# Kernel tuning notes

Hardware: AMD Instinct MI355X
Metric: run time of the kernel (lower is better)

Reference implementation:

```python
import jax, jax.numpy as jnp
import numpy as np

B, N, D, H, HD, C = 2, 2048, 2048, 16, 128, 128  # batch, seq, embed, heads, head_dim, chunk
EPS = 1e-6


def setup_inputs() -> dict:
    key = jax.random.key(0)
    ks = jax.random.split(key, 9)
    s = 0.02
    x = jax.random.normal(ks[0], (B, N, D), jnp.float32)
    # per-head negative log decay (lambda = exp(log_decay) in (0,1))
    log_decay = -jax.random.uniform(ks[1], (H,), jnp.float32, minval=0.01, maxval=1.0)
    Wq = jax.random.normal(ks[2], (D, D), jnp.float32) * s
    Wk = jax.random.normal(ks[3], (D, D), jnp.float32) * s
    Wv = jax.random.normal(ks[4], (D, D), jnp.float32) * s
    Wo = jax.random.normal(ks[5], (D, D), jnp.float32) * s
    Wg1 = jax.random.normal(ks[6], (D, HD), jnp.float32) * s
    Wg2 = jax.random.normal(ks[7], (HD, D), jnp.float32) * s
    norm_w = jnp.ones((D,), jnp.float32)
    return dict(x=x, log_decay=log_decay, Wq=Wq, Wk=Wk, Wv=Wv, Wo=Wo,
                Wg1=Wg1, Wg2=Wg2, norm_w=norm_w)


def _lasd(q, k, v, ld):
    # causal linear attention with per-head scalar log-decay, chunked scan.
    # q,k,v: [B,N,H,HD]; ld: [H] (negative). Recurrence: S_t = exp(ld)*S_{t-1} + k_t v_t^T; o_t = q_t @ S_t
    nc = N // C
    to_chunks = lambda t: t.reshape(B, nc, C, H, HD).transpose(1, 0, 3, 2, 4)  # [nc,B,H,C,HD]
    qc, kc, vc = map(to_chunks, (q, k, v))
    i = jnp.arange(C, dtype=jnp.float32)
    diff = i[:, None] - i[None, :]                     # [C,C]
    Dm = jnp.exp(jnp.where(diff >= 0, ld[:, None, None] * diff, -jnp.inf))  # [H,C,C]
    dq = jnp.exp(ld[:, None] * (i + 1.0))              # [H,C] decay applied to q vs chunk-start state
    dk = jnp.exp(ld[:, None] * (C - 1.0 - i))          # [H,C] decay applied to k for state update
    dS = jnp.exp(ld * C)                               # [H]   chunk-level state decay

    def step(S, qkv):
        qb, kb, vb = qkv                               # [B,H,C,HD]
        attn = jnp.einsum('bhid,bhjd->bhij', qb, kb) * Dm
        o = jnp.einsum('bhij,bhje->bhie', attn, vb)
        o = o + jnp.einsum('bhid,bhde->bhie', qb * dq[None, :, :, None], S)
        S = S * dS[None, :, None, None] + jnp.einsum('bhjd,bhje->bhde', kb * dk[None, :, :, None], vb)
        return S, o

    S0 = jnp.zeros((B, H, HD, HD), jnp.float32)
    _, o = jax.lax.scan(step, S0, (qc, kc, vc))        # [nc,B,H,C,HD]
    return o.transpose(1, 0, 3, 2, 4).reshape(B, N, H, HD)


def reference(x, log_decay, Wq, Wk, Wv, Wo, Wg1, Wg2, norm_w):
    silu = jax.nn.silu
    q = silu(x @ Wq).reshape(B, N, H, HD)
    k = silu(x @ Wk).reshape(B, N, H, HD)
    v = silu(x @ Wv).reshape(B, N, H, HD)
    o = _lasd(q, k, v, log_decay).reshape(B, N, D)
    gate = jax.nn.sigmoid((x @ Wg1) @ Wg2)             # two stacked linears, no nonlinearity between
    o = o * gate
    o = o * jax.lax.rsqrt(jnp.mean(o * o, axis=-1, keepdims=True) + EPS) * norm_w  # rmsnorm
    return o @ Wo
```

## Files before the change

kernel.cpp:

```cpp
#include <hip/hip_runtime.h>
#include <hip/hip_bf16.h>
#include <cstdint>
#include <cstddef>

#define B_   2
#define N_   2048
#define D_   2048
#define H_   16
#define HD_  128
#define C_   128
#define NC_  16
#define M_   4096
#define QKVG_ 8192

typedef __attribute__((ext_vector_type(8))) short bf16x8;
typedef __attribute__((ext_vector_type(4))) float f32x4;
typedef __attribute__((ext_vector_type(16))) float f32x16;

__device__ __forceinline__ uint16_t f2bf(float f){
  __hip_bfloat16 h = __float2bfloat16(f);
  return *reinterpret_cast<uint16_t*>(&h);
}
__device__ __forceinline__ float bf2f(uint16_t u){
  union { uint32_t i; float f; } v; v.i = ((uint32_t)u) << 16; return v.f;
}

__device__ __forceinline__ void async16(const uint16_t* g, uint16_t* l){
  __builtin_amdgcn_global_load_lds(
      (const __attribute__((address_space(1))) void*)g,
      (__attribute__((address_space(3))) void*)l, 16, 0, 0);
}

__device__ __forceinline__ int swz(int row, int c){
  return row*128 + ((((c >> 3) ^ row) & 15) << 3) + (c & 7);
}

__global__ __launch_bounds__(256) void cast_kernel(
    const float* __restrict__ x, uint16_t* __restrict__ y)
{
  int i = (blockIdx.x*256 + threadIdx.x)*4;
  float4 f = *(const float4*)(x + i);
  ushort4 u;
  u.x = f2bf(f.x); u.y = f2bf(f.y); u.z = f2bf(f.z); u.w = f2bf(f.w);
  *(ushort4*)(y + i) = u;
}

__global__ __launch_bounds__(256)
void prep_weights(const float* __restrict__ Wq, const float* __restrict__ Wk,
                  const float* __restrict__ Wv, const float* __restrict__ Wo,
                  const float* __restrict__ Wg2, const float* __restrict__ Wg1,
                  uint16_t* __restrict__ WT, uint16_t* __restrict__ WoT,
                  uint16_t* __restrict__ Wg2T, uint16_t* __restrict__ Wg1b)
{
  const int z = blockIdx.z;
  const int tx = threadIdx.x & 31;
  const int ty = threadIdx.x >> 5;
  __shared__ uint16_t tile[32][33];

  if (z == 5){
    if (blockIdx.x >= 4) return;
    const int r0 = blockIdx.y*32, c0 = blockIdx.x*32;
    #pragma unroll
    for (int rr = 0; rr < 4; ++rr){
      int r = r0 + ty + rr*8;
      Wg1b[(size_t)r*HD_ + c0 + tx] = f2bf(Wg1[(size_t)r*HD_ + c0 + tx]);
    }
    return;
  }

  const float* src; uint16_t* dst; int R, Cc;
  if (z < 3)      { src = (z==0)?Wq:(z==1)?Wk:Wv; dst = WT + (size_t)z*D_*D_; R = D_; Cc = D_; }
  else if (z == 3){ src = Wo;  dst = WoT;  R = D_;  Cc = D_; }
  else            { if (blockIdx.y >= 4) return;
                    src = Wg2; dst = Wg2T; R = HD_; Cc = D_; }

  const int r0 = blockIdx.y*32, c0 = blockIdx.x*32;
  #pragma unroll
  for (int rr = 0; rr < 4; ++rr){
    int r = ty + rr*8;
    tile[r][tx] = f2bf(src[(size_t)(r0 + r)*Cc + c0 + tx]);
  }
  __syncthreads();
  #pragma unroll
  for (int rr = 0; rr < 4; ++rr){
    int r = ty + rr*8;
    dst[(size_t)(c0 + r)*R + r0 + tx] = tile[tx][r];
  }
}

template<int ACT, int OUTBF>
__global__ __launch_bounds__(256)
void gemm_bt2(const uint16_t* __restrict__ A, const uint16_t* __restrict__ Bt,
              void* __restrict__ Cout, int M, int Ncols, int K, int klen)
{
  __shared__ __align__(16) uint16_t As[128*64];
  __shared__ __align__(16) uint16_t Bs[128*64];
  const int t    = threadIdx.x;
  const int lane = t & 63, wave = t >> 6;
  const int wm = wave >> 1, wn = wave & 1;
  const int row0 = wm*64, col0 = wn*64;
  const int lm = lane & 31, lh = lane >> 5;

  const uint16_t* Ap = A  + (size_t)(blockIdx.y*128)*K;
  const uint16_t* Bp = Bt + (size_t)(blockIdx.x*128)*K;
  const int kbeg = blockIdx.z * klen;

  f32x16 acc[2][2];
  #pragma unroll
  for (int i = 0; i < 2; ++i)
    #pragma unroll
    for (int j = 0; j < 2; ++j)
      #pragma unroll
      for (int r = 0; r < 16; ++r) acc[i][j][r] = 0.f;

  const int srow = t >> 3;
  const int gch  = (t & 7) ^ (srow & 7);
  const size_t aoff0 = (size_t)srow*K + gch*8;

  for (int k0 = kbeg; k0 < kbeg + klen; k0 += 64){
    #pragma unroll
    for (int c = 0; c < 4; ++c){
      async16(Ap + (size_t)(c*32)*K + aoff0 + k0, As + c*2048 + t*8);
      async16(Bp + (size_t)(c*32)*K + aoff0 + k0, Bs + c*2048 + t*8);
    }
    __syncthreads();
    #pragma unroll
    for (int kh = 0; kh < 4; ++kh){
      bf16x8 af[2], bfr[2];
      const int ch = kh*2 + lh;
      #pragma unroll
      for (int i = 0; i < 2; ++i){
        int r = row0 + i*32 + lm;
        af[i] = *(const bf16x8*)(As + r*64 + ((ch ^ (r & 7)) << 3));
      }
      #pragma unroll
      for (int j = 0; j < 2; ++j){
        int r = col0 + j*32 + lm;
        bfr[j] = *(const bf16x8*)(Bs + r*64 + ((ch ^ (r & 7)) << 3));
      }
      #pragma unroll
      for (int i = 0; i < 2; ++i)
        #pragma unroll
        for (int j = 0; j < 2; ++j)
          acc[i][j] = __builtin_amdgcn_mfma_f32_32x32x16_bf16(af[i], bfr[j], acc[i][j], 0, 0, 0);
    }
    __syncthreads();
  }

  const int mode = (ACT == 3) ? ((blockIdx.x < 48) ? 1 : 2) : ACT;
  uint16_t* outb = (uint16_t*)Cout;
  float*    outf = (float*)Cout + (OUTBF ? 0 : (size_t)blockIdx.z*M*Ncols);
  #pragma unroll
  for (int i = 0; i < 2; ++i){
    #pragma unroll
    for (int j = 0; j < 2; ++j){
      #pragma unroll
      for (int r = 0; r < 16; ++r){
        int row = blockIdx.y*128 + row0 + i*32 + (r & 3) + 8*(r >> 2) + 4*lh;
        int col = blockIdx.x*128 + col0 + j*32 + lm;
        float v = acc[i][j][r];
        if (mode == 1)      v = v / (1.f + __expf(-v));
        else if (mode == 2) v = 1.f / (1.f + __expf(-v));
        size_t off = (size_t)row*Ncols + col;
        if (OUTBF) outb[off] = f2bf(v);
        else       outf[off] = v;
      }
    }
  }
}

__global__ __launch_bounds__(256)
void add_kernel(const float* __restrict__ p0, const float* __restrict__ p1,
                float* __restrict__ out)
{
  int i = (blockIdx.x*256 + threadIdx.x)*4;
  float4 a = *(const float4*)(p0 + i);
  float4 b = *(const float4*)(p1 + i);
  float4 o; o.x = a.x+b.x; o.y = a.y+b.y; o.z = a.z+b.z; o.w = a.w+b.w;
  *(float4*)(out + i) = o;
}

__global__ __launch_bounds__(256)
void chunk_state_kernel(const uint16_t* __restrict__ qkvg,
                        const float* __restrict__ log_decay, uint16_t* __restrict__ MsumT)
{
  __shared__ __align__(16) uint16_t vT[128*128];
  __shared__ __align__(16) uint16_t kT[128*128];
  const int h = blockIdx.x, b = blockIdx.y, ic = blockIdx.z;
  const int t    = threadIdx.x;
  const int lane = t & 63, wave = t >> 6;
  const int wm = wave >> 1, wn = wave & 1;
  const int e0 = wm*64, d0 = wn*64;
  const int lr = lane & 15, kq = lane >> 4;
  const float ld = log_decay[h];
  const size_t rowbase = (size_t)b*N_ + (size_t)ic*C_;
  const uint16_t* kb = qkvg + (size_t)D_;
  const uint16_t* vb = qkvg + (size_t)2*D_;

  #pragma unroll 4
  for (int it = 0; it < 64; ++it){
    int idx = t + it*256;
    int j = idx >> 7, e = idx & 127;
    uint16_t vv = vb[(rowbase + j)*QKVG_ + h*HD_ + e];
    float kf = bf2f(kb[(rowbase + j)*QKVG_ + h*HD_ + e]) * __expf(ld * (float)(C_ - 1 - j));
    vT[swz(e, j)] = vv;
    kT[swz(e, j)] = f2bf(kf);
  }
  __syncthreads();

  const f32x4 zero = {0.f, 0.f, 0.f, 0.f};
  f32x4 acc[4][4];
  #pragma unroll
  for (int i = 0; i < 4; ++i)
    #pragma unroll
    for (int j = 0; j < 4; ++j) acc[i][j] = zero;

  #pragma unroll
  for (int kt = 0; kt < 4; ++kt){
    bf16x8 af[4], bfr[4];
    #pragma unroll
    for (int i = 0; i < 4; ++i)
      af[i]  = *(const bf16x8*)(vT + swz(e0 + i*16 + lr, kt*32 + kq*8));
    #pragma unroll
    for (int j = 0; j < 4; ++j)
      bfr[j] = *(const bf16x8*)(kT + swz(d0 + j*16 + lr, kt*32 + kq*8));
    #pragma unroll
    for (int i = 0; i < 4; ++i)
      #pragma unroll
      for (int j = 0; j < 4; ++j)
        acc[i][j] = __builtin_amdgcn_mfma_f32_16x16x32_bf16(af[i], bfr[j], acc[i][j], 0, 0, 0);
  }

  uint16_t* Mout = MsumT + (((size_t)ic*B_ + b)*H_ + h)*(size_t)(HD_*HD_);
  #pragma unroll
  for (int i = 0; i < 4; ++i)
    #pragma unroll
    for (int j = 0; j < 4; ++j)
      #pragma unroll
      for (int r = 0; r < 4; ++r)
        Mout[(size_t)(e0 + i*16 + kq*4 + r)*HD_ + d0 + j*16 + lr] = f2bf(acc[i][j][r]);
}

__global__ __launch_bounds__(256)
void scan_kernel(const uint16_t* __restrict__ MsumT, const float* __restrict__ log_decay,
                 uint16_t* __restrict__ StT)
{
  const int h = blockIdx.x, b = blockIdx.y;
  const float ld = log_decay[h];
  const float dS = __expf(ld * (float)C_);
  const int base_e = blockIdx.z*2048;
  float cur[8];
  #pragma unroll
  for (int r = 0; r < 8; ++r) cur[r] = 0.f;
  for (int i = 0; i < NC_; ++i){
    const size_t base = (((size_t)i*B_ + b)*H_ + h)*(size_t)(HD_*HD_) + base_e;
    #pragma unroll
    for (int r = 0; r < 8; ++r){
      int idx = threadIdx.x + r*256;
      StT[base + idx] = f2bf(cur[r]);
      cur[r] = cur[r]*dS + bf2f(MsumT[base + idx]);
    }
  }
}

__global__ __launch_bounds__(256)
void attn_kernel(const uint16_t* __restrict__ qkvg, const uint16_t* __restrict__ StT,
                 const float* __restrict__ log_decay, float* __restrict__ o_attn)
{
  __shared__ __align__(16) uint16_t Ps[128*128];
  __shared__ __align__(16) uint16_t vT[128*128];
  const int h = blockIdx.x, b = blockIdx.y, ic = blockIdx.z;
  const int t    = threadIdx.x;
  const int lane = t & 63, wave = t >> 6;
  const int wm = wave >> 1, wn = wave & 1;
  const int row0 = wm*64, col0 = wn*64;
  const int lr = lane & 15, kq = lane >> 4;
  const float ld = log_decay[h];
  const size_t rowbase = (size_t)b*N_ + (size_t)ic*C_;
  const uint16_t* qb = qkvg;
  const uint16_t* kb = qkvg + (size_t)D_;
  const uint16_t* vb = qkvg + (size_t)2*D_;

  #pragma unroll 4
  for (int it = 0; it < 64; ++it){
    int idx = t + it*256;
    int j = idx >> 7, e = idx & 127;
    vT[swz(e, j)] = vb[(rowbase + j)*QKVG_ + h*HD_ + e];
  }

  const f32x4 zero = {0.f, 0.f, 0.f, 0.f};
  f32x4 acc[4][4];
  #pragma unroll
  for (int i = 0; i < 4; ++i)
    #pragma unroll
    for (int j = 0; j < 4; ++j) acc[i][j] = zero;

  #pragma unroll
  for (int kt = 0; kt < 4; ++kt){
    bf16x8 af[4], bfr[4];
    #pragma unroll
    for (int i = 0; i < 4; ++i)
      af[i]  = *(const bf16x8*)(qb + (rowbase + row0 + i*16 + lr)*QKVG_ + h*HD_ + kt*32 + kq*8);
    #pragma unroll
    for (int j = 0; j < 4; ++j)
      bfr[j] = *(const bf16x8*)(kb + (rowbase + col0 + j*16 + lr)*QKVG_ + h*HD_ + kt*32 + kq*8);
    #pragma unroll
    for (int i = 0; i < 4; ++i)
      #pragma unroll
      for (int j = 0; j < 4; ++j)
        acc[i][j] = __builtin_amdgcn_mfma_f32_16x16x32_bf16(af[i], bfr[j], acc[i][j], 0, 0, 0);
  }
  #pragma unroll
  for (int i = 0; i < 4; ++i)
    #pragma unroll
    for (int j = 0; j < 4; ++j)
      #pragma unroll
      for (int r = 0; r < 4; ++r){
        int row = row0 + i*16 + kq*4 + r;
        int col = col0 + j*16 + lr;
        int dlt = row - col;
        float f = (dlt >= 0) ? __expf(ld * (float)dlt) : 0.f;
        Ps[swz(row, col)] = f2bf(acc[i][j][r] * f);
      }

  #pragma unroll
  for (int i = 0; i < 4; ++i)
    #pragma unroll
    for (int j = 0; j < 4; ++j) acc[i][j] = zero;
  const uint16_t* Sb = StT + (((size_t)ic*B_ + b)*H_ + h)*(size_t)(HD_*HD_);
  #pragma unroll
  for (int kt = 0; kt < 4; ++kt){
    bf16x8 af[4], bfr[4];
    #pragma unroll
    for (int i = 0; i < 4; ++i)
      af[i]  = *(const bf16x8*)(qb + (rowbase + row0 + i*16 + lr)*QKVG_ + h*HD_ + kt*32 + kq*8);
    #pragma unroll
    for (int j = 0; j < 4; ++j)
      bfr[j] = *(const bf16x8*)(Sb + (size_t)(col0 + j*16 + lr)*HD_ + kt*32 + kq*8);
    #pragma unroll
    for (int i = 0; i < 4; ++i)
      #pragma unroll
      for (int j = 0; j < 4; ++j)
        acc[i][j] = __builtin_amdgcn_mfma_f32_16x16x32_bf16(af[i], bfr[j], acc[i][j], 0, 0, 0);
  }
  #pragma unroll
  for (int i = 0; i < 4; ++i)
    #pragma unroll
    for (int r = 0; r < 4; ++r){
      float dqv = __expf(ld * (float)(row0 + i*16 + kq*4 + r + 1));
      #pragma unroll
      for (int j = 0; j < 4; ++j) acc[i][j][r] *= dqv;
    }

  __syncthreads();

  #pragma unroll
  for (int kt = 0; kt < 4; ++kt){
    bf16x8 af[4], bfr[4];
    #pragma unroll
    for (int i = 0; i < 4; ++i)
      af[i]  = *(const bf16x8*)(Ps + swz(row0 + i*16 + lr, kt*32 + kq*8));
    #pragma unroll
    for (int j = 0; j < 4; ++j)
      bfr[j] = *(const bf16x8*)(vT + swz(col0 + j*16 + lr, kt*32 + kq*8));
    #pragma unroll
    for (int i = 0; i < 4; ++i)
      #pragma unroll
      for (int j = 0; j < 4; ++j)
        acc[i][j] = __builtin_amdgcn_mfma_f32_16x16x32_bf16(af[i], bfr[j], acc[i][j], 0, 0, 0);
  }

  #pragma unroll
  for (int i = 0; i < 4; ++i)
    #pragma unroll
    for (int j = 0; j < 4; ++j)
      #pragma unroll
      for (int r = 0; r < 4; ++r){
        int row = row0 + i*16 + kq*4 + r;
        int col = col0 + j*16 + lr;
        o_attn[(rowbase + row)*D_ + h*HD_ + col] = acc[i][j][r];
      }
}

__global__ __launch_bounds__(256)
void gate_norm_kernel(const float* __restrict__ o_attn, const uint16_t* __restrict__ qkvg,
                      const float* __restrict__ norm_w, uint16_t* __restrict__ on)
{
  const int row = blockIdx.x;
  const int t = threadIdx.x;
  const int c1 = t*4, c2 = 1024 + t*4;
  const float*    orow = o_attn + (size_t)row*D_;
  const uint16_t* grow = qkvg + (size_t)row*QKVG_ + 3*D_;
  float4  o1 = *(const float4*)(orow + c1);
  float4  o2 = *(const float4*)(orow + c2);
  ushort4 g1 = *(const ushort4*)(grow + c1);
  ushort4 g2 = *(const ushort4*)(grow + c2);
  float v[8];
  v[0] = o1.x*bf2f(g1.x); v[1] = o1.y*bf2f(g1.y); v[2] = o1.z*bf2f(g1.z); v[3] = o1.w*bf2f(g1.w);
  v[4] = o2.x*bf2f(g2.x); v[5] = o2.y*bf2f(g2.y); v[6] = o2.z*bf2f(g2.z); v[7] = o2.w*bf2f(g2.w);
  float s = 0.f;
  #pragma unroll
  for (int k = 0; k < 8; ++k) s += v[k]*v[k];
  #pragma unroll
  for (int off = 32; off > 0; off >>= 1) s += __shfl_down(s, off);
  __shared__ float red[4];
  if ((t & 63) == 0) red[t >> 6] = s;
  __syncthreads();
  float total = red[0] + red[1] + red[2] + red[3];
  float scale = rsqrtf(total * (1.f/(float)D_) + 1e-6f);
  float4 w1 = *(const float4*)(norm_w + c1);
  float4 w2 = *(const float4*)(norm_w + c2);
  ushort4 b1, b2;
  b1.x = f2bf(v[0]*scale*w1.x); b1.y = f2bf(v[1]*scale*w1.y);
  b1.z = f2bf(v[2]*scale*w1.z); b1.w = f2bf(v[3]*scale*w1.w);
  b2.x = f2bf(v[4]*scale*w2.x); b2.y = f2bf(v[5]*scale*w2.y);
  b2.z = f2bf(v[6]*scale*w2.z); b2.w = f2bf(v[7]*scale*w2.w);
  *(ushort4*)(on + (size_t)row*D_ + c1) = b1;
  *(ushort4*)(on + (size_t)row*D_ + c2) = b2;
}

extern "C" void kernel_launch(void* const* d_in, const int* in_sizes, int n_in,
                              void* d_out, int out_size, void* d_ws, size_t ws_size,
                              hipStream_t stream) {
  const float* x         = (const float*)d_in[0];
  const float* log_decay = (const float*)d_in[1];
  const float* Wq        = (const float*)d_in[2];
  const float* Wk        = (const float*)d_in[3];
  const float* Wv        = (const float*)d_in[4];
  const float* Wo        = (const float*)d_in[5];
  const float* Wg1       = (const float*)d_in[6];
  const float* Wg2       = (const float*)d_in[7];
  const float* norm_w    = (const float*)d_in[8];
  float* out = (float*)d_out;

  uint8_t* p = (uint8_t*)d_ws;
  uint16_t* xb    = (uint16_t*)p; p += (size_t)M_*D_*2;
  uint16_t* WT    = (uint16_t*)p; p += (size_t)QKVG_*D_*2;
  uint16_t* WoT   = (uint16_t*)p; p += (size_t)D_*D_*2;
  uint16_t* Wg1b  = (uint16_t*)p; p += (size_t)D_*HD_*2;
  uint16_t* Wg2T  = (uint16_t*)p; p += (size_t)D_*HD_*2;
  uint16_t* qkvg  = (uint16_t*)p; p += (size_t)M_*QKVG_*2;
  uint16_t* MsumT = (uint16_t*)p; p += (size_t)NC_*B_*H_*HD_*HD_*2;
  uint16_t* StT   = (uint16_t*)p; p += (size_t)NC_*B_*H_*HD_*HD_*2;
  float*    o_att = (float*)WT;
  uint16_t* on    = xb;
  float*    part  = (float*)qkvg;

  cast_kernel<<<(M_*D_)/1024, 256, 0, stream>>>(x, xb);
  prep_weights<<<dim3(64, 64, 6), 256, 0, stream>>>(Wq, Wk, Wv, Wo, Wg2, Wg1,
                                                    WT, WoT, Wg2T, Wg1b);

  gemm_bt2<0,1><<<dim3(D_/128, D_/128, 1), 256, 0, stream>>>(
      Wg2T, Wg1b, WT + (size_t)3*D_*D_, D_, D_, HD_, HD_);

  gemm_bt2<3,1><<<dim3(QKVG_/128, M_/128, 1), 256, 0, stream>>>(
      xb, WT, qkvg, M_, QKVG_, D_, D_);

  chunk_state_kernel<<<dim3(H_, B_, NC_), 256, 0, stream>>>(qkvg, log_decay, MsumT);
  scan_kernel<<<dim3(H_, B_, 8), 256, 0, stream>>>(MsumT, log_decay, StT);
  attn_kernel<<<dim3(H_, B_, NC_), 256, 0, stream>>>(qkvg, StT, log_decay, o_att);

  gate_norm_kernel<<<M_, 256, 0, stream>>>(o_att, qkvg, norm_w, on);
  gemm_bt2<0,0><<<dim3(D_/128, M_/128, 2), 256, 0, stream>>>(
      on, WoT, part, M_, D_, D_, D_/2);
  add_kernel<<<(M_*D_)/1024, 256, 0, stream>>>(part, part + (size_t)M_*D_, out);
}
```

Before: 426.3 us.

## Add 256x256-tile double-buffered GEMM and use it for QKVG and output projections

After: 480.2 us. 12.6% more time.

```diff
diff --git a/kernel.cpp b/kernel.cpp
--- a/kernel.cpp
+++ b/kernel.cpp
@@ -158,6 +158,128 @@
       for (int r = 0; r < 16; ++r){
         int row = blockIdx.y*128 + row0 + i*32 + (r & 3) + 8*(r >> 2) + 4*lh;
         int col = blockIdx.x*128 + col0 + j*32 + lm;
+        float v = acc[i][j][r];
+        if (mode == 1)      v = v / (1.f + __expf(-v));
+        else if (mode == 2) v = 1.f / (1.f + __expf(-v));
+        size_t off = (size_t)row*Ncols + col;
+        if (OUTBF) outb[off] = f2bf(v);
+        else       outf[off] = v;
+      }
+    }
+  }
+}
+
+template<int ACT, int OUTBF>
+__global__ __launch_bounds__(512, 2)
+void gemm256(const uint16_t* __restrict__ A, const uint16_t* __restrict__ Bt,
+             void* __restrict__ Cout, int M, int Ncols, int K, int klen)
+{
+  __shared__ __align__(16) uint16_t As[2*256*32];
+  __shared__ __align__(16) uint16_t Bs[2*256*32];
+  const int t    = threadIdx.x;
+  const int lane = t & 63, wave = t >> 6;
+  const int wm = wave >> 1, wn = wave & 1;
+  const int lm = lane & 31, lh = lane >> 5;
+  const int sl0 = (lh ^ (lm & 3)) << 3;
+  const int ar = wm*64  + lm;
+  const int br = wn*128 + lm;
+
+  const uint16_t* Ap = A  + (size_t)(blockIdx.y*256)*K;
+  const uint16_t* Bp = Bt + (size_t)(blockIdx.x*256)*K;
+  const int kbeg = blockIdx.z*klen;
+  const int NT   = klen >> 5;
+
+  const int r_lo = t >> 2;
+  const int gch  = (t & 3) ^ (r_lo & 3);
+  const size_t src0 = (size_t)r_lo*K + gch*8;
+  const size_t src1 = src0 + (size_t)128*K;
+  const int ldst = t*8;
+
+  f32x16 acc[2][4];
+  #pragma unroll
+  for (int i = 0; i < 2; ++i)
+    #pragma unroll
+    for (int j = 0; j < 4; ++j)
+      #pragma unroll
+      for (int r = 0; r < 16; ++r) acc[i][j][r] = 0.f;
+
+  async16(Ap + src0 + kbeg,      As + ldst);
+  async16(Ap + src1 + kbeg,      As + 4096 + ldst);
+  async16(Bp + src0 + kbeg,      Bs + ldst);
+  async16(Bp + src1 + kbeg,      Bs + 4096 + ldst);
+  async16(Ap + src0 + kbeg + 32, As + 8192 + ldst);
+  async16(Ap + src1 + kbeg + 32, As + 8192 + 4096 + ldst);
+  async16(Bp + src0 + kbeg + 32, Bs + 8192 + ldst);
+  async16(Bp + src1 + kbeg + 32, Bs + 8192 + 4096 + ldst);
+  asm volatile("s_waitcnt vmcnt(4)" ::: "memory");
+  __builtin_amdgcn_s_barrier();
+  asm volatile("" ::: "memory");
+
+  bf16x8 af0[2], bf0[4], af1[2], bf1[4];
+  #pragma unroll
+  for (int i = 0; i < 2; ++i) af0[i] = *(const bf16x8*)(As + (ar + i*32)*32 + sl0);
+  #pragma unroll
+  for (int j = 0; j < 4; ++j) bf0[j] = *(const bf16x8*)(Bs + (br + j*32)*32 + sl0);
+
+  for (int tt = 0; tt < NT; ++tt){
+    uint16_t* Ac = As + (tt & 1)*8192;
+    uint16_t* Bc = Bs + (tt & 1)*8192;
+    const uint16_t* An = As + ((tt & 1) ^ 1)*8192;
+    const uint16_t* Bn = Bs + ((tt & 1) ^ 1)*8192;
+
+    #pragma unroll
+    for (int i = 0; i < 2; ++i) af1[i] = *(const bf16x8*)(Ac + (ar + i*32)*32 + (sl0 ^ 16));
+    #pragma unroll
+    for (int j = 0; j < 4; ++j) bf1[j] = *(const bf16x8*)(Bc + (br + j*32)*32 + (sl0 ^ 16));
+    __builtin_amdgcn_s_setprio(1);
+    #pragma unroll
+    for (int i = 0; i < 2; ++i)
+      #pragma unroll
+      for (int j = 0; j < 4; ++j)
+        acc[i][j] = __builtin_amdgcn_mfma_f32_32x32x16_bf16(af0[i], bf0[j], acc[i][j], 0, 0, 0);
+    __builtin_amdgcn_s_setprio(0);
+    asm volatile("s_waitcnt lgkmcnt(0)" ::: "memory");
+    __builtin_amdgcn_s_barrier();
+    asm volatile("" ::: "memory");
+
+    if (tt + 2 < NT){
+      const size_t kc = (size_t)kbeg + (size_t)(tt + 2)*32;
+      async16(Ap + src0 + kc, Ac + ldst);
+      async16(Ap + src1 + kc, Ac + 4096 + ldst);
+      async16(Bp + src0 + kc, Bc + ldst);
+      async16(Bp + src1 + kc, Bc + 4096 + ldst);
+      asm volatile("s_waitcnt vmcnt(4)" ::: "memory");
+    } else {
+      asm volatile("s_waitcnt vmcnt(0)" ::: "memory");
+    }
+    __builtin_amdgcn_s_barrier();
+    asm volatile("" ::: "memory");
+    if (tt + 1 < NT){
+      #pragma unroll
+      for (int i = 0; i < 2; ++i) af0[i] = *(const bf16x8*)(An + (ar + i*32)*32 + sl0);
+      #pragma unroll
+      for (int j = 0; j < 4; ++j) bf0[j] = *(const bf16x8*)(Bn + (br + j*32)*32 + sl0);
+    }
+    __builtin_amdgcn_s_setprio(1);
+    #pragma unroll
+    for (int i = 0; i < 2; ++i)
+      #pragma unroll
+      for (int j = 0; j < 4; ++j)
+        acc[i][j] = __builtin_amdgcn_mfma_f32_32x32x16_bf16(af1[i], bf1[j], acc[i][j], 0, 0, 0);
+    __builtin_amdgcn_s_setprio(0);
+  }
+
+  const int mode = (ACT == 3) ? (((blockIdx.x << 8) < Ncols - 2048) ? 1 : 2) : ACT;
+  uint16_t* outb = (uint16_t*)Cout;
+  float*    outf = (float*)Cout + (OUTBF ? 0 : (size_t)blockIdx.z*M*Ncols);
+  #pragma unroll
+  for (int i = 0; i < 2; ++i){
+    #pragma unroll
+    for (int j = 0; j < 4; ++j){
+      #pragma unroll
+      for (int r = 0; r < 16; ++r){
+        int row = blockIdx.y*256 + wm*64  + i*32 + (r & 3) + 8*(r >> 2) + 4*lh;
+        int col = blockIdx.x*256 + wn*128 + j*32 + lm;
         float v = acc[i][j][r];
         if (mode == 1)      v = v / (1.f + __expf(-v));
         else if (mode == 2) v = 1.f / (1.f + __expf(-v));
@@ -453,7 +575,7 @@
   gemm_bt2<0,1><<<dim3(D_/128, D_/128, 1), 256, 0, stream>>>(
       Wg2T, Wg1b, WT + (size_t)3*D_*D_, D_, D_, HD_, HD_);
 
-  gemm_bt2<3,1><<<dim3(QKVG_/128, M_/128, 1), 256, 0, stream>>>(
+  gemm256<3,1><<<dim3(QKVG_/256, M_/256, 1), 512, 0, stream>>>(
       xb, WT, qkvg, M_, QKVG_, D_, D_);
 
   chunk_state_kernel<<<dim3(H_, B_, NC_), 256, 0, stream>>>(qkvg, log_decay, MsumT);
@@ -461,7 +583,7 @@
   attn_kernel<<<dim3(H_, B_, NC_), 256, 0, stream>>>(qkvg, StT, log_decay, o_att);
 
   gate_norm_kernel<<<M_, 256, 0, stream>>>(o_att, qkvg, norm_w, on);
-  gemm_bt2<0,0><<<dim3(D_/128, M_/128, 2), 256, 0, stream>>>(
+  gemm256<0,0><<<dim3(D_/256, M_/256, 2), 512, 0, stream>>>(
       on, WoT, part, M_, D_, D_, D_/2);
   add_kernel<<<(M_*D_)/1024, 256, 0, stream>>>(part, part + (size_t)M_*D_, out);
 }
```
